# Performance work log

Hardware: AMD Instinct MI355X
Metric: run time of the kernel (lower is better)

## Reference

```python
import jax, jax.numpy as jnp
import numpy as np


def setup_inputs() -> dict:
    key = jax.random.key(0)
    k1, k2 = jax.random.split(key)
    B, H, W, C = 8, 512, 512, 32
    img = jax.random.normal(k1, (B, H, W, C), dtype=jnp.float32)
    # normalized coords in [-1, 1]
    grid = jax.random.uniform(k2, (B, H, W, 2), dtype=jnp.float32, minval=-1.0, maxval=1.0)
    return {"img": img, "grid": grid}


def reference(img, grid):
    B, H, W, C = img.shape
    max_y = H - 1
    max_x = W - 1
    # unnormalize from [-1,1] to pixel coords
    x = 0.5 * ((grid[..., 0] + 1.0) * jnp.float32(max_x))
    y = 0.5 * ((grid[..., 1] + 1.0) * jnp.float32(max_y))

    x0 = jnp.floor(x).astype(jnp.int32)
    x1 = x0 + 1
    y0 = jnp.floor(y).astype(jnp.int32)
    y1 = y0 + 1

    x0c = jnp.clip(x0, 0, max_x)
    x1c = jnp.clip(x1, 0, max_x)
    y0c = jnp.clip(y0, 0, max_y)
    y1c = jnp.clip(y1, 0, max_y)

    b = jnp.arange(B, dtype=jnp.int32)[:, None, None]  # [B,1,1], broadcasts over grid HxW

    Ia = img[b, y0c, x0c]  # [B,Hg,Wg,C]
    Ib = img[b, y1c, x0c]
    Ic = img[b, y0c, x1c]
    Id = img[b, y1c, x1c]

    x0f = x0c.astype(jnp.float32)
    x1f = x1c.astype(jnp.float32)
    y0f = y0c.astype(jnp.float32)
    y1f = y1c.astype(jnp.float32)

    wa = ((x1f - x) * (y1f - y))[..., None]
    wb = ((x1f - x) * (y - y0f))[..., None]
    wc = ((x - x0f) * (y1f - y))[..., None]
    wd = ((x - x0f) * (y - y0f))[..., None]

    return wa * Ia + wb * Ib + wc * Ic + wd * Id
```

## Files before the change

### kernel.cpp

```cpp
#include <hip/hip_runtime.h>


#define NBINS 128u
#define CAP   20480u
#define ENT_OFF 4096

__device__ __forceinline__ void bilinear_px(
    const float* __restrict__ ibase,
    float* __restrict__ out, unsigned pix, float x, float y, unsigned c)
{
    const int x0 = (int)floorf(x);
    const int y0 = (int)floorf(y);
    const int x0c = min(max(x0,     0), 511);
    const int x1c = min(max(x0 + 1, 0), 511);
    const int y0c = min(max(y0,     0), 511);
    const int y1c = min(max(y0 + 1, 0), 511);

    const float4 Ia = *reinterpret_cast<const float4*>(ibase + (unsigned)(y0c*512 + x0c)*32u + c);
    const float4 Ic = *reinterpret_cast<const float4*>(ibase + (unsigned)(y0c*512 + x1c)*32u + c);
    const float4 Ib = *reinterpret_cast<const float4*>(ibase + (unsigned)(y1c*512 + x0c)*32u + c);
    const float4 Id = *reinterpret_cast<const float4*>(ibase + (unsigned)(y1c*512 + x1c)*32u + c);

    const float wa = ((float)x1c - x) * ((float)y1c - y);
    const float wb = ((float)x1c - x) * (y - (float)y0c);
    const float wc = (x - (float)x0c) * ((float)y1c - y);
    const float wd = (x - (float)x0c) * (y - (float)y0c);

    float4 o;
    o.x = wa*Ia.x + wb*Ib.x + wc*Ic.x + wd*Id.x;
    o.y = wa*Ia.y + wb*Ib.y + wc*Ic.y + wd*Id.y;
    o.z = wa*Ia.z + wb*Ib.z + wc*Ic.z + wd*Id.z;
    o.w = wa*Ia.w + wb*Ib.w + wc*Ic.w + wd*Id.w;
    *reinterpret_cast<float4*>(out + (size_t)pix*32u + c) = o;
}

__global__ __launch_bounds__(256) void gs_bin(
    const float* __restrict__ grid,
    const float* __restrict__ img,
    float* __restrict__ out,
    unsigned* __restrict__ gcnt,
    float4* __restrict__ entries)
{
    __shared__ unsigned lcnt[16];
    __shared__ unsigned lbase[16];
    const unsigned tid = threadIdx.x;
    if (tid < 16) lcnt[tid] = 0;
    __syncthreads();

    const unsigned blockbase = blockIdx.x << 10;
    const unsigned batch = blockbase >> 18;

    float xs[4], ys[4];
    unsigned bandk[4], slotk[4], pixk[4];
    #pragma unroll
    for (int k = 0; k < 4; ++k) {
        const unsigned pix = blockbase + tid + ((unsigned)k << 8);
        const float2 g = *reinterpret_cast<const float2*>(grid + (size_t)pix * 2u);
        const float x = 0.5f * ((g.x + 1.0f) * 511.0f);
        const float y = 0.5f * ((g.y + 1.0f) * 511.0f);
        const int y0 = (int)floorf(y);
        const int y0c = min(max(y0, 0), 511);
        const unsigned band = (unsigned)y0c >> 5;
        slotk[k] = atomicAdd(&lcnt[band], 1u);
        bandk[k] = band; pixk[k] = pix; xs[k] = x; ys[k] = y;
    }
    __syncthreads();
    if (tid < 16) lbase[tid] = atomicAdd(&gcnt[batch * 16u + tid], lcnt[tid]);
    __syncthreads();

    const float* ibase = img + (((size_t)batch << 18) * 32u);
    #pragma unroll
    for (int k = 0; k < 4; ++k) {
        const unsigned idx = lbase[bandk[k]] + slotk[k];
        const unsigned bin = batch * 16u + bandk[k];
        if (idx < CAP) {
            float4 e;
            e.x = xs[k]; e.y = ys[k];
            e.z = __uint_as_float(pixk[k]); e.w = 0.0f;
            entries[(size_t)bin * CAP + idx] = e;
        } else {
            for (unsigned c = 0; c < 32; c += 4)
                bilinear_px(ibase, out, pixk[k], xs[k], ys[k], c);
        }
    }
}

__global__ __launch_bounds__(256) void gs_apply(
    const float* __restrict__ img,
    float* __restrict__ out,
    const unsigned* __restrict__ gcnt,
    const float4* __restrict__ entries)
{
    const unsigned bid = blockIdx.x;
    const unsigned xcd      = bid & 7u;
    const unsigned j        = bid >> 3;
    const unsigned ord      = j >> 9;
    const unsigned blkInBin = j & 511u;
    const unsigned bin   = ord * 8u + xcd;
    const unsigned batch = bin >> 4;

    unsigned n = gcnt[bin];
    if (n > CAP) n = CAP;

    const unsigned tid = threadIdx.x;
    const unsigned grp = tid >> 3;
    const unsigned c   = (tid & 7u) << 2;
    const float* ibase = img + (((size_t)batch << 18) * 32u);

    for (unsigned p = blkInBin * 32u + grp; p < n; p += 16384u) {
        const float4 e = entries[(size_t)bin * CAP + p];
        bilinear_px(ibase, out, __float_as_uint(e.z), e.x, e.y, c);
    }
}

__global__ __launch_bounds__(256) void gs_direct(
    const float* __restrict__ img,
    const float* __restrict__ grid,
    float* __restrict__ out)
{
    const unsigned gid = blockIdx.x * 256u + threadIdx.x;
    const unsigned pix = gid >> 3;
    const unsigned c   = (gid & 7u) << 2;
    const float2 g = *reinterpret_cast<const float2*>(grid + (size_t)pix * 2u);
    const float x = 0.5f * ((g.x + 1.0f) * 511.0f);
    const float y = 0.5f * ((g.y + 1.0f) * 511.0f);
    const unsigned batch = pix >> 18;
    const float* ibase = img + (((size_t)batch << 18) * 32u);
    bilinear_px(ibase, out, pix, x, y, c);
}

extern "C" void kernel_launch(void* const* d_in, const int* in_sizes, int n_in,
                              void* d_out, int out_size, void* d_ws, size_t ws_size,
                              hipStream_t stream) {
    const float* img  = (const float*)d_in[0];
    const float* grid = (const float*)d_in[1];
    float* out = (float*)d_out;

    const size_t need = (size_t)ENT_OFF + (size_t)NBINS * CAP * sizeof(float4);
    if (d_ws != nullptr && ws_size >= need) {
        unsigned* gcnt  = (unsigned*)d_ws;
        float4* entries = (float4*)((char*)d_ws + ENT_OFF);
        hipMemsetAsync(gcnt, 0, NBINS * sizeof(unsigned), stream);
        gs_bin<<<2048, 256, 0, stream>>>(grid, img, out, gcnt, entries);
        gs_apply<<<65536, 256, 0, stream>>>(img, out, gcnt, entries);
    } else {
        gs_direct<<<65536, 256, 0, stream>>>(img, grid, out);
    }
}
```

Before: 501.8 us.

## Bin samples into fine 2x128 tiles and gather from LDS-staged image tiles

Replaces the coarse 16-band-per-batch binning with 8192 fine bins, each covering 2 rows by 128 columns, using direct global atomics per sample. The apply kernel stages each bin's 3x129-pixel image patch in shared memory and gathers all four bilinear taps from LDS, with nontemporal output stores. Entries are split into separate xy and pixel arrays. The aim is to replace scattered global gathers with one coalesced tile load per bin; the cost is heavy global atomic contention, a per-bin CAP of 352 that sends overflowing samples down the slow direct path, and about 50 KB of LDS per block, which limits occupancy.

```diff
diff --git a/kernel.cpp b/kernel.cpp
--- a/kernel.cpp
+++ b/kernel.cpp
@@ -1,9 +1,13 @@
 #include <hip/hip_runtime.h>
 
 
-#define NBINS 128u
-#define CAP   20480u
-#define ENT_OFF 4096
+#define NBINS   8192u
+#define CAP     352u
+#define EXY_OFF 32768u
+#define EPIX_OFF (32768u + 8192u*352u*8u)
+#define WS_NEED ((size_t)EPIX_OFF + (size_t)8192u*352u*4u)
+
+typedef float f4_t __attribute__((ext_vector_type(4)));
 
 __device__ __forceinline__ void bilinear_px(
     const float* __restrict__ ibase,
@@ -39,77 +43,104 @@
     const float* __restrict__ img,
     float* __restrict__ out,
     unsigned* __restrict__ gcnt,
-    float4* __restrict__ entries)
+    float2* __restrict__ exy,
+    unsigned* __restrict__ epix)
 {
-    __shared__ unsigned lcnt[16];
-    __shared__ unsigned lbase[16];
     const unsigned tid = threadIdx.x;
-    if (tid < 16) lcnt[tid] = 0;
-    __syncthreads();
-
     const unsigned blockbase = blockIdx.x << 10;
     const unsigned batch = blockbase >> 18;
+    const float* ibase = img + (((size_t)batch << 18) * 32u);
 
-    float xs[4], ys[4];
-    unsigned bandk[4], slotk[4], pixk[4];
     #pragma unroll
     for (int k = 0; k < 4; ++k) {
         const unsigned pix = blockbase + tid + ((unsigned)k << 8);
         const float2 g = *reinterpret_cast<const float2*>(grid + (size_t)pix * 2u);
         const float x = 0.5f * ((g.x + 1.0f) * 511.0f);
         const float y = 0.5f * ((g.y + 1.0f) * 511.0f);
-        const int y0 = (int)floorf(y);
-        const int y0c = min(max(y0, 0), 511);
-        const unsigned band = (unsigned)y0c >> 5;
-        slotk[k] = atomicAdd(&lcnt[band], 1u);
-        bandk[k] = band; pixk[k] = pix; xs[k] = x; ys[k] = y;
-    }
-    __syncthreads();
-    if (tid < 16) lbase[tid] = atomicAdd(&gcnt[batch * 16u + tid], lcnt[tid]);
-    __syncthreads();
-
-    const float* ibase = img + (((size_t)batch << 18) * 32u);
-    #pragma unroll
-    for (int k = 0; k < 4; ++k) {
-        const unsigned idx = lbase[bandk[k]] + slotk[k];
-        const unsigned bin = batch * 16u + bandk[k];
-        if (idx < CAP) {
-            float4 e;
-            e.x = xs[k]; e.y = ys[k];
-            e.z = __uint_as_float(pixk[k]); e.w = 0.0f;
-            entries[(size_t)bin * CAP + idx] = e;
+        const int x0c = min(max((int)floorf(x), 0), 511);
+        const int y0c = min(max((int)floorf(y), 0), 511);
+        const unsigned bin = (batch << 10) | (((unsigned)y0c >> 1) << 2) | ((unsigned)x0c >> 7);
+        const unsigned slot = atomicAdd(&gcnt[bin], 1u);
+        if (slot < CAP) {
+            exy[(size_t)bin * CAP + slot]  = make_float2(x, y);
+            epix[(size_t)bin * CAP + slot] = pix;
         } else {
             for (unsigned c = 0; c < 32; c += 4)
-                bilinear_px(ibase, out, pixk[k], xs[k], ys[k], c);
+                bilinear_px(ibase, out, pix, x, y, c);
         }
     }
 }
 
-__global__ __launch_bounds__(256) void gs_apply(
+__global__ __launch_bounds__(256) void gs_tile(
     const float* __restrict__ img,
     float* __restrict__ out,
     const unsigned* __restrict__ gcnt,
-    const float4* __restrict__ entries)
+    const float2* __restrict__ exy,
+    const unsigned* __restrict__ epix)
 {
-    const unsigned bid = blockIdx.x;
-    const unsigned xcd      = bid & 7u;
-    const unsigned j        = bid >> 3;
-    const unsigned ord      = j >> 9;
-    const unsigned blkInBin = j & 511u;
-    const unsigned bin   = ord * 8u + xcd;
-    const unsigned batch = bin >> 4;
+    __shared__ float tile[3 * 129 * 32];
+
+    const unsigned bid  = blockIdx.x;
+    const unsigned bin  = (bid & 7u) * 1024u + (bid >> 3);
+    const unsigned batch = bin >> 10;
+    const unsigned yband = (bin >> 2) & 255u;
+    const unsigned xband = bin & 3u;
+    const int r0 = (int)(yband << 1);
+    const int c0 = (int)(xband << 7);
+    const unsigned tid = threadIdx.x;
+
+    const float* ib = img + (((size_t)batch << 18) * 32u);
+    float4* t4 = reinterpret_cast<float4*>(tile);
+    for (unsigned f = tid; f < 3096u; f += 256u) {
+        const unsigned l   = f >> 3;
+        const unsigned sub = f & 7u;
+        const unsigned row = l / 129u;
+        const unsigned col = l - row * 129u;
+        const int gr = min(r0 + (int)row, 511);
+        const int gc = min(c0 + (int)col, 511);
+        t4[f] = *reinterpret_cast<const float4*>(ib + (unsigned)(gr*512 + gc)*32u + (sub << 2));
+    }
+    __syncthreads();
 
     unsigned n = gcnt[bin];
     if (n > CAP) n = CAP;
 
-    const unsigned tid = threadIdx.x;
     const unsigned grp = tid >> 3;
     const unsigned c   = (tid & 7u) << 2;
-    const float* ibase = img + (((size_t)batch << 18) * 32u);
+    const size_t  base = (size_t)bin * CAP;
 
-    for (unsigned p = blkInBin * 32u + grp; p < n; p += 16384u) {
-        const float4 e = entries[(size_t)bin * CAP + p];
-        bilinear_px(ibase, out, __float_as_uint(e.z), e.x, e.y, c);
+    for (unsigned p = grp; p < n; p += 32u) {
+        const float2 e  = exy[base + p];
+        const unsigned pix = epix[base + p];
+        const float x = e.x, y = e.y;
+
+        const int x0 = (int)floorf(x);
+        const int y0 = (int)floorf(y);
+        const int x0c = min(max(x0,     0), 511);
+        const int x1c = min(max(x0 + 1, 0), 511);
+        const int y0c = min(max(y0,     0), 511);
+        const int y1c = min(max(y0 + 1, 0), 511);
+
+        const int lx0 = x0c - c0, lx1 = x1c - c0;
+        const int ly0 = y0c - r0, ly1 = y1c - r0;
+
+        const float4 Ia = *reinterpret_cast<const float4*>(tile + (unsigned)((ly0*129 + lx0) << 5) + c);
+        const float4 Ic = *reinterpret_cast<const float4*>(tile + (unsigned)((ly0*129 + lx1) << 5) + c);
+        const float4 Ib = *reinterpret_cast<const float4*>(tile + (unsigned)((ly1*129 + lx0) << 5) + c);
+        const float4 Id = *reinterpret_cast<const float4*>(tile + (unsigned)((ly1*129 + lx1) << 5) + c);
+
+        const float wa = ((float)x1c - x) * ((float)y1c - y);
+        const float wb = ((float)x1c - x) * (y - (float)y0c);
+        const float wc = (x - (float)x0c) * ((float)y1c - y);
+        const float wd = (x - (float)x0c) * (y - (float)y0c);
+
+        f4_t o;
+        o.x = wa*Ia.x + wb*Ib.x + wc*Ic.x + wd*Id.x;
+        o.y = wa*Ia.y + wb*Ib.y + wc*Ic.y + wd*Id.y;
+        o.z = wa*Ia.z + wb*Ib.z + wc*Ic.z + wd*Id.z;
+        o.w = wa*Ia.w + wb*Ib.w + wc*Ic.w + wd*Id.w;
+
+        __builtin_nontemporal_store(o, reinterpret_cast<f4_t*>(out + (size_t)pix*32u + c));
     }
 }
 
@@ -136,13 +167,13 @@
     const float* grid = (const float*)d_in[1];
     float* out = (float*)d_out;
 
-    const size_t need = (size_t)ENT_OFF + (size_t)NBINS * CAP * sizeof(float4);
-    if (d_ws != nullptr && ws_size >= need) {
-        unsigned* gcnt  = (unsigned*)d_ws;
-        float4* entries = (float4*)((char*)d_ws + ENT_OFF);
+    if (d_ws != nullptr && ws_size >= WS_NEED) {
+        unsigned* gcnt = (unsigned*)d_ws;
+        float2*   exy  = (float2*)((char*)d_ws + EXY_OFF);
+        unsigned* epix = (unsigned*)((char*)d_ws + EPIX_OFF);
         hipMemsetAsync(gcnt, 0, NBINS * sizeof(unsigned), stream);
-        gs_bin<<<2048, 256, 0, stream>>>(grid, img, out, gcnt, entries);
-        gs_apply<<<65536, 256, 0, stream>>>(img, out, gcnt, entries);
+        gs_bin<<<2048, 256, 0, stream>>>(grid, img, out, gcnt, exy, epix);
+        gs_tile<<<NBINS, 256, 0, stream>>>(img, out, gcnt, exy, epix);
     } else {
         gs_direct<<<65536, 256, 0, stream>>>(img, grid, out);
     }
```

Measured after the change: 636.2 us. +26.8%, slower.

## Bin only half the pixels and fuse direct sampling with binned apply

Applied to the files above, without the earlier changes.

The binning kernel now sorts only half of each 2048-pixel chunk into row-band bins, with a smaller per-bin capacity. A fused kernel interleaves blocks that process the binned entries with blocks that sample the remaining pixels directly from the grid. This is meant to cut the write and read traffic of the entry buffer and the binning cost, at the price of poorer cache locality for the directly processed half.

```diff
diff --git a/kernel.cpp b/kernel.cpp
--- a/kernel.cpp
+++ b/kernel.cpp
@@ -1,9 +1,10 @@
 #include <hip/hip_runtime.h>
 
 
-#define NBINS 128u
-#define CAP   20480u
+#define NBINS  128u
+#define CAP    9472u
 #define ENT_OFF 4096
+#define WS_NEED ((size_t)ENT_OFF + (size_t)NBINS * CAP * sizeof(float4))
 
 __device__ __forceinline__ void bilinear_px(
     const float* __restrict__ ibase,
@@ -34,7 +35,7 @@
     *reinterpret_cast<float4*>(out + (size_t)pix*32u + c) = o;
 }
 
-__global__ __launch_bounds__(256) void gs_bin(
+__global__ __launch_bounds__(256) void gs_binh(
     const float* __restrict__ grid,
     const float* __restrict__ img,
     float* __restrict__ out,
@@ -47,19 +48,20 @@
     if (tid < 16) lcnt[tid] = 0;
     __syncthreads();
 
-    const unsigned blockbase = blockIdx.x << 10;
-    const unsigned batch = blockbase >> 18;
+    const unsigned scbase = blockIdx.x << 11;
+    const unsigned batch  = scbase >> 18;
 
     float xs[4], ys[4];
     unsigned bandk[4], slotk[4], pixk[4];
     #pragma unroll
     for (int k = 0; k < 4; ++k) {
-        const unsigned pix = blockbase + tid + ((unsigned)k << 8);
+        const unsigned off = (k < 2) ? (512u + (unsigned)k * 256u)
+                                     : (1024u + 512u + (unsigned)(k - 2) * 256u);
+        const unsigned pix = scbase + off + tid;
         const float2 g = *reinterpret_cast<const float2*>(grid + (size_t)pix * 2u);
         const float x = 0.5f * ((g.x + 1.0f) * 511.0f);
         const float y = 0.5f * ((g.y + 1.0f) * 511.0f);
-        const int y0 = (int)floorf(y);
-        const int y0c = min(max(y0, 0), 511);
+        const int y0c = min(max((int)floorf(y), 0), 511);
         const unsigned band = (unsigned)y0c >> 5;
         slotk[k] = atomicAdd(&lcnt[band], 1u);
         bandk[k] = band; pixk[k] = pix; xs[k] = x; ys[k] = y;
@@ -85,31 +87,45 @@
     }
 }
 
-__global__ __launch_bounds__(256) void gs_apply(
+__global__ __launch_bounds__(256) void gs_fused(
     const float* __restrict__ img,
+    const float* __restrict__ grid,
     float* __restrict__ out,
     const unsigned* __restrict__ gcnt,
     const float4* __restrict__ entries)
 {
     const unsigned bid = blockIdx.x;
-    const unsigned xcd      = bid & 7u;
-    const unsigned j        = bid >> 3;
-    const unsigned ord      = j >> 9;
-    const unsigned blkInBin = j & 511u;
-    const unsigned bin   = ord * 8u + xcd;
-    const unsigned batch = bin >> 4;
-
-    unsigned n = gcnt[bin];
-    if (n > CAP) n = CAP;
-
+    const unsigned g   = bid >> 4;
+    const unsigned r   = bid & 15u;
     const unsigned tid = threadIdx.x;
     const unsigned grp = tid >> 3;
     const unsigned c   = (tid & 7u) << 2;
-    const float* ibase = img + (((size_t)batch << 18) * 32u);
 
-    for (unsigned p = blkInBin * 32u + grp; p < n; p += 16384u) {
-        const float4 e = entries[(size_t)bin * CAP + p];
-        bilinear_px(ibase, out, __float_as_uint(e.z), e.x, e.y, c);
+    if (r < 8u) {
+        const unsigned ord      = g >> 8;
+        const unsigned blkInBin = g & 255u;
+        const unsigned bin      = ord * 8u + r;
+        const unsigned batch    = bin >> 4;
+
+        unsigned n = gcnt[bin];
+        if (n > CAP) n = CAP;
+
+        const float* ibase = img + (((size_t)batch << 18) * 32u);
+        const size_t  base = (size_t)bin * CAP;
+
+        for (unsigned p = blkInBin * 32u + grp; p < n; p += 8192u) {
+            const float4 e = entries[base + p];
+            bilinear_px(ibase, out, __float_as_uint(e.z), e.x, e.y, c);
+        }
+    } else {
+        const unsigned d = g * 8u + (r - 8u);
+        const unsigned pix = (d >> 4) * 1024u + (d & 15u) * 32u + grp;
+        const float2 gg = *reinterpret_cast<const float2*>(grid + (size_t)pix * 2u);
+        const float x = 0.5f * ((gg.x + 1.0f) * 511.0f);
+        const float y = 0.5f * ((gg.y + 1.0f) * 511.0f);
+        const unsigned batch = pix >> 18;
+        const float* ibase = img + (((size_t)batch << 18) * 32u);
+        bilinear_px(ibase, out, pix, x, y, c);
     }
 }
 
@@ -136,13 +152,12 @@
     const float* grid = (const float*)d_in[1];
     float* out = (float*)d_out;
 
-    const size_t need = (size_t)ENT_OFF + (size_t)NBINS * CAP * sizeof(float4);
-    if (d_ws != nullptr && ws_size >= need) {
+    if (d_ws != nullptr && ws_size >= WS_NEED) {
         unsigned* gcnt  = (unsigned*)d_ws;
         float4* entries = (float4*)((char*)d_ws + ENT_OFF);
         hipMemsetAsync(gcnt, 0, NBINS * sizeof(unsigned), stream);
-        gs_bin<<<2048, 256, 0, stream>>>(grid, img, out, gcnt, entries);
-        gs_apply<<<65536, 256, 0, stream>>>(img, out, gcnt, entries);
+        gs_binh<<<1024, 256, 0, stream>>>(grid, img, out, gcnt, entries);
+        gs_fused<<<65536, 256, 0, stream>>>(img, grid, out, gcnt, entries);
     } else {
         gs_direct<<<65536, 256, 0, stream>>>(img, grid, out);
     }
```

Result: no change. 505.0 us (+0.6%).
